# Performance work log

Measured on AMD Instinct MI355X. Metric: run time of the kernel, lower is better.

## Reference

```python
import jax, jax.numpy as jnp
import numpy as np

HIDDEN = 2048
LATENT = 512
ROPE_DIM = 64
NUM_HEADS = 16
HEAD_DIM = HIDDEN // NUM_HEADS  # 128
ROPE_THETA = 10000.0
B, S = 2, 2048


def _rope_tables(seq_len):
    # theta_i = 1 / rope_theta ** (2i / rope_dim)
    theta = 1.0 / ROPE_THETA ** (jnp.arange(0, ROPE_DIM, 2, dtype=jnp.float32) / ROPE_DIM)
    idx_theta = jnp.arange(seq_len, dtype=jnp.float32)[:, None] * theta[None, :]  # [S, rd/2]
    return jnp.cos(idx_theta), jnp.sin(idx_theta)


def _apply_rope(x, cos, sin):
    # x: [B, S, H, rd]; interleaved pairs rotated, matching the torch RoPE module.
    x2 = x.reshape(*x.shape[:-1], -1, 2)  # [B,S,H,rd/2,2]
    c = cos[None, :, None, :]
    s = sin[None, :, None, :]
    out = jnp.stack([x2[..., 0] * c - x2[..., 1] * s,
                     x2[..., 1] * c + x2[..., 0] * s], axis=-1)
    return out.reshape(x.shape)


def setup_inputs() -> dict:
    key = jax.random.key(0)
    ks = jax.random.split(key, 9)
    def lin(k, fan_in, fan_out):
        # weights stored [in, out]; y = x @ W (same math as torch Linear)
        bound = 1.0 / np.sqrt(fan_in)
        return jax.random.uniform(k, (fan_in, fan_out), jnp.float32, -bound, bound)
    return {
        "h": jax.random.normal(ks[0], (B, S, HIDDEN), jnp.float32),
        "W_DKV": lin(ks[1], HIDDEN, LATENT),
        "W_UK": lin(ks[2], LATENT, HIDDEN),
        "W_KR": lin(ks[3], HIDDEN, ROPE_DIM),
        "W_UV": lin(ks[4], LATENT, HIDDEN),
        "W_DQ": lin(ks[5], HIDDEN, LATENT),
        "W_UQ": lin(ks[6], LATENT, HIDDEN),
        "W_QR": lin(ks[7], LATENT, ROPE_DIM * NUM_HEADS),
        "W_O": lin(ks[8], HIDDEN, HIDDEN),
    }


def reference(h, W_DKV, W_UK, W_KR, W_UV, W_DQ, W_UQ, W_QR, W_O):
    b, s, _ = h.shape
    cos, sin = _rope_tables(s)

    # --- keys / values (shared latent) ---
    c_KV = h @ W_DKV                                      # [B,S,latent]
    k_C = (c_KV @ W_UK).reshape(b, s, NUM_HEADS, HEAD_DIM)
    k_R = _apply_rope((h @ W_KR)[:, :, None, :], cos, sin)  # [B,S,1,rd]
    k_R = jnp.broadcast_to(k_R, (b, s, NUM_HEADS, ROPE_DIM))
    k = jnp.concatenate([k_C, k_R], axis=-1)             # [B,S,H,hd+rd]
    v = (c_KV @ W_UV).reshape(b, s, NUM_HEADS, HEAD_DIM)

    # --- queries ---
    c_Q = h @ W_DQ                                        # [B,S,latent]
    q_C = (c_Q @ W_UQ).reshape(b, s, NUM_HEADS, HEAD_DIM)
    q_R = _apply_rope((c_Q @ W_QR).reshape(b, s, NUM_HEADS, ROPE_DIM), cos, sin)
    q = jnp.concatenate([q_C, q_R], axis=-1)             # [B,S,H,hd+rd]

    # --- attention (explicit SxS scores, causal) ---
    scale = 1.0 / np.sqrt(HEAD_DIM + ROPE_DIM)
    scores = jnp.einsum('bshd,bthd->bhst', q, k) * scale  # [B,H,S,S]
    causal = jnp.tril(jnp.ones((s, s), dtype=bool))
    scores = jnp.where(causal[None, None], scores, -jnp.inf)
    probs = jax.nn.softmax(scores, axis=-1)
    o = jnp.einsum('bhst,bthd->bshd', probs, v)           # [B,S,H,hd]

    return o.reshape(b, s, HIDDEN) @ W_O
```

## Files before the change

### kernel.cpp

```cpp
#include <hip/hip_runtime.h>
#include <hip/hip_bf16.h>
#include <type_traits>
#include <cstdint>

typedef __bf16 bf16x8 __attribute__((ext_vector_type(8)));
typedef float f32x4 __attribute__((ext_vector_type(4)));
typedef __hip_bfloat16 bf16;

static constexpr int BB = 2, SEQ = 2048, HID = 2048, LAT = 512, NHEAD = 16;
static constexpr int HD = 128, RD = 64, DQK = 192;
static constexpr int MR = BB * SEQ;
static constexpr int LDW1 = 1152;
static constexpr int LDKV = 4096;
static constexpr int LDQ3 = 3072;

__device__ __forceinline__ float bf2f(bf16 x) { return __bfloat162float(x); }
__device__ __forceinline__ bf16 f2bf(float x) { return __float2bfloat16(x); }

__device__ __forceinline__ void gload16(const void* g, void* l) {
  __builtin_amdgcn_global_load_lds(
      (__attribute__((address_space(1))) void*)(uintptr_t)g,
      (__attribute__((address_space(3))) void*)(uint32_t)(uintptr_t)l,
      16, 0, 0);
}

__global__ void k_cvt(const float* __restrict__ in, bf16* __restrict__ out, int n4) {
  int i = blockIdx.x * 256 + threadIdx.x;
  if (i >= n4) return;
  float4 v = reinterpret_cast<const float4*>(in)[i];
  bf16* o = out + (size_t)i * 4;
  o[0] = f2bf(v.x); o[1] = f2bf(v.y); o[2] = f2bf(v.z); o[3] = f2bf(v.w);
}

__global__ void k_transpose_cvt(const float* __restrict__ W, bf16* __restrict__ WT,
                                int K, int N) {
  __shared__ float t[32][33];
  int k0 = blockIdx.y * 32, n0 = blockIdx.x * 32;
  int c = threadIdx.x & 31, r0 = threadIdx.x >> 5;
#pragma unroll
  for (int i = 0; i < 32; i += 8) t[r0 + i][c] = W[(size_t)(k0 + r0 + i) * N + n0 + c];
  __syncthreads();
#pragma unroll
  for (int i = 0; i < 32; i += 8)
    WT[(size_t)(n0 + r0 + i) * K + k0 + c] = f2bf(t[c][r0 + i]);
}

__global__ void k_transpose_v(const bf16* __restrict__ kv, bf16* __restrict__ vt) {
  __shared__ bf16 t[32][34];
  int bh = blockIdx.z, b = bh >> 4, hh = bh & 15;
  int s0 = blockIdx.y * 32, d0 = blockIdx.x * 32;
  int c = threadIdx.x & 31, r0 = threadIdx.x >> 5;
#pragma unroll
  for (int i = 0; i < 32; i += 8)
    t[r0 + i][c] = kv[((size_t)b * SEQ + s0 + r0 + i) * LDKV + HID + hh * HD + d0 + c];
  __syncthreads();
#pragma unroll
  for (int i = 0; i < 32; i += 8)
    vt[((size_t)bh * HD + d0 + r0 + i) * SEQ + s0 + c] = t[c][r0 + i];
}

__global__ void k_rope_tables(float* __restrict__ cosT, float* __restrict__ sinT) {
  int idx = blockIdx.x * 256 + threadIdx.x;
  int s = idx >> 5, j = idx & 31;
  float freq = powf(10000.0f, -(float)(2 * j) / 64.0f);
  float a = (float)s * freq;
  cosT[idx] = cosf(a);
  sinT[idx] = sinf(a);
}

template <int BM, int BN, typename OutT>
__global__ __launch_bounds__((BM / 64) * (BN / 64) * 64)
void k_gemm_bt(const bf16* __restrict__ A, int lda, const bf16* __restrict__ BT,
               OutT* __restrict__ C, int ldc, int M, int N, int K) {
  constexpr int BK = 32;
  constexpr int WN = BN / 64, NW = (BM / 64) * WN;
  __shared__ alignas(16) bf16 As[BM * BK];
  __shared__ alignas(16) bf16 Bs[BN * BK];
  const int tid = threadIdx.x, wave = tid >> 6, lane = tid & 63;
  const int lr = lane & 15, lk = lane >> 4;
  const int wm = (wave / WN) * 64, wn = (wave % WN) * 64;
  const int m0 = blockIdx.y * BM, n0 = blockIdx.x * BN;
  const int srow = lane >> 2;
  const int scol = (lane & 3) * 8;
  f32x4 acc[4][4] = {};
  for (int kt = 0; kt < K; kt += BK) {
    for (int c = wave; c < BM / 16; c += NW)
      gload16(A + (size_t)(m0 + c * 16 + srow) * lda + kt + scol, (char*)As + c * 1024);
    for (int c = wave; c < BN / 16; c += NW)
      gload16(BT + (size_t)(n0 + c * 16 + srow) * K + kt + scol, (char*)Bs + c * 1024);
    __syncthreads();
    bf16x8 af[4], bfr[4];
#pragma unroll
    for (int i = 0; i < 4; i++)
      af[i] = *reinterpret_cast<const bf16x8*>(As + (wm + i * 16 + lr) * BK + lk * 8);
#pragma unroll
    for (int j = 0; j < 4; j++)
      bfr[j] = *reinterpret_cast<const bf16x8*>(Bs + (wn + j * 16 + lr) * BK + lk * 8);
    __builtin_amdgcn_s_setprio(1);
#pragma unroll
    for (int i = 0; i < 4; i++)
#pragma unroll
      for (int j = 0; j < 4; j++)
        acc[i][j] = __builtin_amdgcn_mfma_f32_16x16x32_bf16(af[i], bfr[j], acc[i][j], 0, 0, 0);
    __builtin_amdgcn_s_setprio(0);
    __syncthreads();
  }
#pragma unroll
  for (int i = 0; i < 4; i++)
#pragma unroll
    for (int j = 0; j < 4; j++) {
      int row = m0 + wm + i * 16 + lk * 4, col = n0 + wn + j * 16 + lr;
#pragma unroll
      for (int r = 0; r < 4; r++) {
        float v = acc[i][j][r];
        if constexpr (std::is_same<OutT, float>::value)
          C[(size_t)(row + r) * ldc + col] = v;
        else
          C[(size_t)(row + r) * ldc + col] = f2bf(v);
      }
    }
}

__global__ void k_assemble_q(const bf16* __restrict__ q3,
                             const float* __restrict__ cosT, const float* __restrict__ sinT,
                             bf16* __restrict__ qbuf) {
  size_t idx = (size_t)blockIdx.x * 256 + threadIdx.x;
  int d = (int)(idx % DQK);
  size_t t = idx / DQK;
  int s = (int)(t % SEQ); t /= SEQ;
  int hh = (int)(t % NHEAD);
  int b = (int)(t / NHEAD);
  size_t row = (size_t)b * SEQ + s;
  bf16 v;
  if (d < HD) {
    v = q3[row * LDQ3 + hh * HD + d];
  } else {
    int dd = d - HD, j = dd >> 1;
    float cs = cosT[s * 32 + j], sn = sinT[s * 32 + j];
    float x0 = bf2f(q3[row * LDQ3 + HID + hh * RD + 2 * j]);
    float x1 = bf2f(q3[row * LDQ3 + HID + hh * RD + 2 * j + 1]);
    v = f2bf((dd & 1) ? (x1 * cs + x0 * sn) : (x0 * cs - x1 * sn));
  }
  qbuf[idx] = v;
}

__global__ void k_assemble_k(const bf16* __restrict__ kv, const bf16* __restrict__ out1,
                             const float* __restrict__ cosT, const float* __restrict__ sinT,
                             bf16* __restrict__ kbuf) {
  size_t idx = (size_t)blockIdx.x * 256 + threadIdx.x;
  int d = (int)(idx % DQK);
  size_t t = idx / DQK;
  int s = (int)(t % SEQ); t /= SEQ;
  int hh = (int)(t % NHEAD);
  int b = (int)(t / NHEAD);
  size_t row = (size_t)b * SEQ + s;
  bf16 v;
  if (d < HD) {
    v = kv[row * LDKV + hh * HD + d];
  } else {
    int dd = d - HD, j = dd >> 1;
    float cs = cosT[s * 32 + j], sn = sinT[s * 32 + j];
    float x0 = bf2f(out1[row * LDW1 + 1024 + 2 * j]);
    float x1 = bf2f(out1[row * LDW1 + 1024 + 2 * j + 1]);
    v = f2bf((dd & 1) ? (x1 * cs + x0 * sn) : (x0 * cs - x1 * sn));
  }
  kbuf[idx] = v;
}

__global__ __launch_bounds__(256)
void k_attn(const bf16* __restrict__ Q, const bf16* __restrict__ Kb,
            const bf16* __restrict__ VT, bf16* __restrict__ Of) {
  constexpr int QB = 64, KBL = 64;
  __shared__ alignas(16) bf16 Ks[KBL * DQK];
  __shared__ alignas(16) bf16 Vs[HD * KBL];
  __shared__ alignas(16) bf16 Ps[4 * 16 * KBL];
  const int qt = (SEQ / QB - 1) - (blockIdx.x >> 5);
  const int bh = blockIdx.x & 31;
  const int b = bh >> 4, hh = bh & 15;
  const int tid = threadIdx.x, wave = tid >> 6, lane = tid & 63;
  const int lr = lane & 15, lk = lane >> 4;
  const int q0 = qt * QB;
  const float scale = 0.07216878364870323f;

  const bf16* Qp = Q + ((size_t)bh * SEQ + q0 + wave * 16 + lr) * DQK;
  bf16x8 qf[6];
#pragma unroll
  for (int c = 0; c < 6; c++)
    qf[c] = *reinterpret_cast<const bf16x8*>(Qp + c * 32 + lk * 8);

  bf16* PsW = Ps + wave * (16 * KBL);

  f32x4 oacc[8] = {};
  float mrow[4], lrow[4];
#pragma unroll
  for (int r = 0; r < 4; r++) { mrow[r] = -INFINITY; lrow[r] = 0.f; }

  for (int kt = 0; kt <= qt; kt++) {
    const int k0 = kt * KBL;
    const bf16* Kbase = Kb + ((size_t)bh * SEQ + k0) * DQK;
    const bf16* Vbase = VT + (size_t)bh * HD * SEQ + k0;
    for (int c = wave; c < 24; c += 4) {
      int S = c * 64 + lane;
      int row = S / 24;
      int scl = (S - row * 24) ^ (row & 7);
      gload16(Kbase + row * DQK + scl * 8, (char*)Ks + c * 1024);
    }
    for (int c = wave; c < 16; c += 4) {
      int S = c * 64 + lane;
      int row = S >> 3;
      int scl = (S & 7) ^ (row & 7);
      gload16(Vbase + (size_t)row * SEQ + scl * 8, (char*)Vs + c * 1024);
    }
    __syncthreads();

    f32x4 sc[4] = {};
    __builtin_amdgcn_s_setprio(1);
#pragma unroll
    for (int cb = 0; cb < 4; cb++) {
      const int krow = cb * 16 + lr;
#pragma unroll
      for (int c = 0; c < 6; c++) {
        int phys = (c * 4 + lk) ^ (krow & 7);
        bf16x8 kf = *reinterpret_cast<const bf16x8*>(Ks + krow * DQK + phys * 8);
        sc[cb] = __builtin_amdgcn_mfma_f32_16x16x32_bf16(qf[c], kf, sc[cb], 0, 0, 0);
      }
    }
    __builtin_amdgcn_s_setprio(0);

    const bool maskit = (kt == qt);
    float p[4][4], tm[4];
#pragma unroll
    for (int r = 0; r < 4; r++) tm[r] = -INFINITY;
#pragma unroll
    for (int cb = 0; cb < 4; cb++) {
      const int kcg = k0 + cb * 16 + lr;
#pragma unroll
      for (int r = 0; r < 4; r++) {
        float v = sc[cb][r] * scale;
        if (maskit && kcg > q0 + wave * 16 + lk * 4 + r) v = -INFINITY;
        p[cb][r] = v;
        tm[r] = fmaxf(tm[r], v);
      }
    }
#pragma unroll
    for (int m = 1; m < 16; m <<= 1)
#pragma unroll
      for (int r = 0; r < 4; r++) tm[r] = fmaxf(tm[r], __shfl_xor(tm[r], m, 16));

    float rs[4];
#pragma unroll
    for (int r = 0; r < 4; r++) {
      float mn = fmaxf(mrow[r], tm[r]);
      float al = __expf(mrow[r] - mn);
      mrow[r] = mn;
      lrow[r] *= al;
#pragma unroll
      for (int ocb = 0; ocb < 8; ocb++) oacc[ocb][r] *= al;
      float ssum = 0.f;
#pragma unroll
      for (int cb = 0; cb < 4; cb++) {
        float e = __expf(p[cb][r] - mn);
        p[cb][r] = e;
        ssum += e;
      }
      rs[r] = ssum;
    }
#pragma unroll
    for (int m = 1; m < 16; m <<= 1)
#pragma unroll
      for (int r = 0; r < 4; r++) rs[r] += __shfl_xor(rs[r], m, 16);
#pragma unroll
    for (int r = 0; r < 4; r++) lrow[r] += rs[r];

#pragma unroll
    for (int cb = 0; cb < 4; cb++)
#pragma unroll
      for (int r = 0; r < 4; r++) {
        int prow = lk * 4 + r;
        int pslot = (cb * 2 + (lr >> 3)) ^ (prow & 7);
        PsW[prow * KBL + pslot * 8 + (lr & 7)] = f2bf(p[cb][r]);
      }

    __builtin_amdgcn_s_setprio(1);
#pragma unroll
    for (int kk = 0; kk < 2; kk++) {
      int pphys = (kk * 4 + lk) ^ (lr & 7);
      bf16x8 pa = *reinterpret_cast<const bf16x8*>(PsW + lr * KBL + pphys * 8);
#pragma unroll
      for (int ocb = 0; ocb < 8; ocb++) {
        int vrow = ocb * 16 + lr;
        int vphys = (kk * 4 + lk) ^ (vrow & 7);
        bf16x8 vb = *reinterpret_cast<const bf16x8*>(Vs + vrow * KBL + vphys * 8);
        oacc[ocb] = __builtin_amdgcn_mfma_f32_16x16x32_bf16(pa, vb, oacc[ocb], 0, 0, 0);
      }
    }
    __builtin_amdgcn_s_setprio(0);
    __syncthreads();
  }

#pragma unroll
  for (int ocb = 0; ocb < 8; ocb++)
#pragma unroll
    for (int r = 0; r < 4; r++) {
      int qr = q0 + wave * 16 + lk * 4 + r;
      float v = oacc[ocb][r] / lrow[r];
      Of[((size_t)b * SEQ + qr) * HID + hh * HD + ocb * 16 + lr] = f2bf(v);
    }
}

extern "C" void kernel_launch(void* const* d_in, const int* in_sizes, int n_in,
                              void* d_out, int out_size, void* d_ws, size_t ws_size,
                              hipStream_t stream) {
  const float* h    = (const float*)d_in[0];
  const float* Wdkv = (const float*)d_in[1];
  const float* Wuk  = (const float*)d_in[2];
  const float* Wkr  = (const float*)d_in[3];
  const float* Wuv  = (const float*)d_in[4];
  const float* Wdq  = (const float*)d_in[5];
  const float* Wuq  = (const float*)d_in[6];
  const float* Wqr  = (const float*)d_in[7];
  const float* Wo   = (const float*)d_in[8];
  float* out = (float*)d_out;

  char* w = (char*)d_ws;
  auto alloc = [&](size_t elems) {
    bf16* p = (bf16*)w;
    w += (elems * sizeof(bf16) + 255) & ~(size_t)255;
    return p;
  };
  bf16* hb   = alloc((size_t)MR * HID);
  bf16* wt1  = alloc((size_t)LDW1 * HID);
  bf16* wt2  = alloc((size_t)LDKV * LAT);
  bf16* wt3  = alloc((size_t)LDQ3 * LAT);
  bf16* woT  = alloc((size_t)HID * HID);
  bf16* out1 = alloc((size_t)MR * LDW1);
  bf16* kv   = alloc((size_t)MR * LDKV);
  bf16* q3   = alloc((size_t)MR * LDQ3);
  bf16* qbuf = alloc((size_t)BB * NHEAD * SEQ * DQK);
  bf16* kbuf = alloc((size_t)BB * NHEAD * SEQ * DQK);
  bf16* vt   = alloc((size_t)BB * NHEAD * HD * SEQ);
  bf16* oflat= alloc((size_t)MR * HID);
  float* cosT = (float*)alloc((size_t)SEQ * 32 * 2);
  float* sinT = (float*)alloc((size_t)SEQ * 32 * 2);

  k_cvt<<<MR * HID / 4 / 256, 256, 0, stream>>>(h, hb, MR * HID / 4);
  k_transpose_cvt<<<dim3(512 / 32, HID / 32), 256, 0, stream>>>(Wdkv, wt1, HID, 512);
  k_transpose_cvt<<<dim3(512 / 32, HID / 32), 256, 0, stream>>>(Wdq, wt1 + (size_t)512 * HID, HID, 512);
  k_transpose_cvt<<<dim3(RD / 32, HID / 32), 256, 0, stream>>>(Wkr, wt1 + (size_t)1024 * HID, HID, RD);
  k_transpose_cvt<<<dim3(HID / 32, LAT / 32), 256, 0, stream>>>(Wuk, wt2, LAT, HID);
  k_transpose_cvt<<<dim3(HID / 32, LAT / 32), 256, 0, stream>>>(Wuv, wt2 + (size_t)HID * LAT, LAT, HID);
  k_transpose_cvt<<<dim3(HID / 32, LAT / 32), 256, 0, stream>>>(Wuq, wt3, LAT, HID);
  k_transpose_cvt<<<dim3(RD * NHEAD / 32, LAT / 32), 256, 0, stream>>>(Wqr, wt3 + (size_t)HID * LAT, LAT, RD * NHEAD);
  k_transpose_cvt<<<dim3(HID / 32, HID / 32), 256, 0, stream>>>(Wo, woT, HID, HID);
  k_rope_tables<<<SEQ * 32 / 256, 256, 0, stream>>>(cosT, sinT);

  k_gemm_bt<128, 128, bf16><<<dim3(LDW1 / 128, MR / 128), 256, 0, stream>>>(hb, HID, wt1, out1, LDW1, MR, LDW1, HID);
  k_gemm_bt<128, 128, bf16><<<dim3(LDKV / 128, MR / 128), 256, 0, stream>>>(out1, LDW1, wt2, kv, LDKV, MR, LDKV, LAT);
  k_gemm_bt<128, 128, bf16><<<dim3(LDQ3 / 128, MR / 128), 256, 0, stream>>>(out1 + 512, LDW1, wt3, q3, LDQ3, MR, LDQ3, LAT);

  unsigned qblocks = (unsigned)((size_t)BB * NHEAD * SEQ * DQK / 256);
  k_assemble_q<<<qblocks, 256, 0, stream>>>(q3, cosT, sinT, qbuf);
  k_assemble_k<<<qblocks, 256, 0, stream>>>(kv, out1, cosT, sinT, kbuf);
  k_transpose_v<<<dim3(HD / 32, SEQ / 32, BB * NHEAD), 256, 0, stream>>>(kv, vt);

  k_attn<<<(SEQ / 64) * 32, 256, 0, stream>>>(qbuf, kbuf, vt, oflat);

  k_gemm_bt<128, 128, float><<<dim3(HID / 128, MR / 128), 256, 0, stream>>>(oflat, HID, woT, out, HID, MR, HID, HID);
}
```

Baseline: 470.0 us.

## Merge prep/assemble launches, fuse kv/q GEMMs, pair causal q-tiles in attention

Folds the weight transposes, h conversion and rope table build into one prep kernel, and merges the two latent-up GEMMs into one launch. Q/K assembly plus the V transpose become a single kernel with 8-wide vector loads and stores. The attention kernel now gives each block two query tiles, one early and one late, so causal work is balanced across blocks and each loaded K/V tile is used twice. It also skips the softmax rescale when the running max does not change. This cuts launch count and load imbalance at the cost of more registers in attention (two sets of accumulators) and fewer attention blocks.

```diff
diff --git a/kernel.cpp b/kernel.cpp
--- a/kernel.cpp
+++ b/kernel.cpp
@@ -24,54 +24,58 @@
       16, 0, 0);
 }
 
-__global__ void k_cvt(const float* __restrict__ in, bf16* __restrict__ out, int n4) {
-  int i = blockIdx.x * 256 + threadIdx.x;
-  if (i >= n4) return;
-  float4 v = reinterpret_cast<const float4*>(in)[i];
-  bf16* o = out + (size_t)i * 4;
-  o[0] = f2bf(v.x); o[1] = f2bf(v.y); o[2] = f2bf(v.z); o[3] = f2bf(v.w);
-}
-
-__global__ void k_transpose_cvt(const float* __restrict__ W, bf16* __restrict__ WT,
-                                int K, int N) {
-  __shared__ float t[32][33];
-  int k0 = blockIdx.y * 32, n0 = blockIdx.x * 32;
+__global__ void k_prep(const float* __restrict__ h,
+                       const float* __restrict__ Wdkv, const float* __restrict__ Wdq,
+                       const float* __restrict__ Wkr, const float* __restrict__ Wuk,
+                       const float* __restrict__ Wuv, const float* __restrict__ Wuq,
+                       const float* __restrict__ Wqr, const float* __restrict__ Wo,
+                       bf16* __restrict__ hb, bf16* __restrict__ wt1, bf16* __restrict__ wt2,
+                       bf16* __restrict__ wt3, bf16* __restrict__ woT,
+                       float* __restrict__ cosT, float* __restrict__ sinT) {
+  __shared__ float tbuf[32][33];
+  int blk = blockIdx.x;
+  if (blk >= 10112) {
+    int i = (blk - 10112) * 256 + threadIdx.x;
+    float4 v = reinterpret_cast<const float4*>(h)[i];
+    bf16* o = hb + (size_t)i * 4;
+    o[0] = f2bf(v.x); o[1] = f2bf(v.y); o[2] = f2bf(v.z); o[3] = f2bf(v.w);
+    return;
+  }
+  if (blk >= 9856) {
+    int idx = (blk - 9856) * 256 + threadIdx.x;
+    int s = idx >> 5, j = idx & 31;
+    float freq = powf(10000.0f, -(float)(2 * j) / 64.0f);
+    float a = (float)s * freq;
+    cosT[idx] = cosf(a);
+    sinT[idx] = sinf(a);
+    return;
+  }
+  const float* src; bf16* dst; int K, N, local;
+  if (blk < 1024)      { src = Wdkv; dst = wt1;                      K = 2048; N = 512;  local = blk; }
+  else if (blk < 2048) { src = Wdq;  dst = wt1 + (size_t)512 * 2048; K = 2048; N = 512;  local = blk - 1024; }
+  else if (blk < 2176) { src = Wkr;  dst = wt1 + (size_t)1024 * 2048;K = 2048; N = 64;   local = blk - 2048; }
+  else if (blk < 3200) { src = Wuk;  dst = wt2;                      K = 512;  N = 2048; local = blk - 2176; }
+  else if (blk < 4224) { src = Wuv;  dst = wt2 + (size_t)2048 * 512; K = 512;  N = 2048; local = blk - 3200; }
+  else if (blk < 5248) { src = Wuq;  dst = wt3;                      K = 512;  N = 2048; local = blk - 4224; }
+  else if (blk < 5760) { src = Wqr;  dst = wt3 + (size_t)2048 * 512; K = 512;  N = 1024; local = blk - 5248; }
+  else                 { src = Wo;   dst = woT;                      K = 2048; N = 2048; local = blk - 5760; }
+  int tilesX = N >> 5;
+  int tx = local % tilesX, ty = local / tilesX;
+  int k0 = ty * 32, n0 = tx * 32;
   int c = threadIdx.x & 31, r0 = threadIdx.x >> 5;
 #pragma unroll
-  for (int i = 0; i < 32; i += 8) t[r0 + i][c] = W[(size_t)(k0 + r0 + i) * N + n0 + c];
+  for (int i = 0; i < 32; i += 8) tbuf[r0 + i][c] = src[(size_t)(k0 + r0 + i) * N + n0 + c];
   __syncthreads();
 #pragma unroll
   for (int i = 0; i < 32; i += 8)
-    WT[(size_t)(n0 + r0 + i) * K + k0 + c] = f2bf(t[c][r0 + i]);
-}
-
-__global__ void k_transpose_v(const bf16* __restrict__ kv, bf16* __restrict__ vt) {
-  __shared__ bf16 t[32][34];
-  int bh = blockIdx.z, b = bh >> 4, hh = bh & 15;
-  int s0 = blockIdx.y * 32, d0 = blockIdx.x * 32;
-  int c = threadIdx.x & 31, r0 = threadIdx.x >> 5;
-#pragma unroll
-  for (int i = 0; i < 32; i += 8)
-    t[r0 + i][c] = kv[((size_t)b * SEQ + s0 + r0 + i) * LDKV + HID + hh * HD + d0 + c];
-  __syncthreads();
-#pragma unroll
-  for (int i = 0; i < 32; i += 8)
-    vt[((size_t)bh * HD + d0 + r0 + i) * SEQ + s0 + c] = t[c][r0 + i];
-}
-
-__global__ void k_rope_tables(float* __restrict__ cosT, float* __restrict__ sinT) {
-  int idx = blockIdx.x * 256 + threadIdx.x;
-  int s = idx >> 5, j = idx & 31;
-  float freq = powf(10000.0f, -(float)(2 * j) / 64.0f);
-  float a = (float)s * freq;
-  cosT[idx] = cosf(a);
-  sinT[idx] = sinf(a);
+    dst[(size_t)(n0 + r0 + i) * K + k0 + c] = f2bf(tbuf[c][r0 + i]);
 }
 
 template <int BM, int BN, typename OutT>
-__global__ __launch_bounds__((BM / 64) * (BN / 64) * 64)
-void k_gemm_bt(const bf16* __restrict__ A, int lda, const bf16* __restrict__ BT,
-               OutT* __restrict__ C, int ldc, int M, int N, int K) {
+__device__ __forceinline__ void gemm_body(const bf16* __restrict__ A, int lda,
+                                          const bf16* __restrict__ BT,
+                                          OutT* __restrict__ C, int ldc, int K,
+                                          int m0, int n0) {
   constexpr int BK = 32;
   constexpr int WN = BN / 64, NW = (BM / 64) * WN;
   __shared__ alignas(16) bf16 As[BM * BK];
@@ -79,7 +83,6 @@
   const int tid = threadIdx.x, wave = tid >> 6, lane = tid & 63;
   const int lr = lane & 15, lk = lane >> 4;
   const int wm = (wave / WN) * 64, wn = (wave % WN) * 64;
-  const int m0 = blockIdx.y * BM, n0 = blockIdx.x * BN;
   const int srow = lane >> 2;
   const int scol = (lane & 3) * 8;
   f32x4 acc[4][4] = {};
@@ -121,81 +124,211 @@
     }
 }
 
-__global__ void k_assemble_q(const bf16* __restrict__ q3,
-                             const float* __restrict__ cosT, const float* __restrict__ sinT,
-                             bf16* __restrict__ qbuf) {
-  size_t idx = (size_t)blockIdx.x * 256 + threadIdx.x;
-  int d = (int)(idx % DQK);
-  size_t t = idx / DQK;
-  int s = (int)(t % SEQ); t /= SEQ;
-  int hh = (int)(t % NHEAD);
-  int b = (int)(t / NHEAD);
-  size_t row = (size_t)b * SEQ + s;
-  bf16 v;
-  if (d < HD) {
-    v = q3[row * LDQ3 + hh * HD + d];
-  } else {
-    int dd = d - HD, j = dd >> 1;
-    float cs = cosT[s * 32 + j], sn = sinT[s * 32 + j];
-    float x0 = bf2f(q3[row * LDQ3 + HID + hh * RD + 2 * j]);
-    float x1 = bf2f(q3[row * LDQ3 + HID + hh * RD + 2 * j + 1]);
-    v = f2bf((dd & 1) ? (x1 * cs + x0 * sn) : (x0 * cs - x1 * sn));
-  }
-  qbuf[idx] = v;
-}
-
-__global__ void k_assemble_k(const bf16* __restrict__ kv, const bf16* __restrict__ out1,
-                             const float* __restrict__ cosT, const float* __restrict__ sinT,
-                             bf16* __restrict__ kbuf) {
-  size_t idx = (size_t)blockIdx.x * 256 + threadIdx.x;
-  int d = (int)(idx % DQK);
-  size_t t = idx / DQK;
-  int s = (int)(t % SEQ); t /= SEQ;
-  int hh = (int)(t % NHEAD);
-  int b = (int)(t / NHEAD);
-  size_t row = (size_t)b * SEQ + s;
-  bf16 v;
-  if (d < HD) {
-    v = kv[row * LDKV + hh * HD + d];
-  } else {
-    int dd = d - HD, j = dd >> 1;
-    float cs = cosT[s * 32 + j], sn = sinT[s * 32 + j];
-    float x0 = bf2f(out1[row * LDW1 + 1024 + 2 * j]);
-    float x1 = bf2f(out1[row * LDW1 + 1024 + 2 * j + 1]);
-    v = f2bf((dd & 1) ? (x1 * cs + x0 * sn) : (x0 * cs - x1 * sn));
-  }
-  kbuf[idx] = v;
+template <int BM, int BN, typename OutT>
+__global__ __launch_bounds__(256)
+void k_gemm_bt(const bf16* __restrict__ A, int lda, const bf16* __restrict__ BT,
+               OutT* __restrict__ C, int ldc, int K) {
+  gemm_body<BM, BN, OutT>(A, lda, BT, C, ldc, K, blockIdx.y * BM, blockIdx.x * BN);
+}
+
+__global__ __launch_bounds__(256)
+void k_gemm23(const bf16* __restrict__ out1, const bf16* __restrict__ wt2,
+              const bf16* __restrict__ wt3, bf16* __restrict__ kv, bf16* __restrict__ q3) {
+  int n0g = blockIdx.x * 128, m0 = blockIdx.y * 128;
+  const bf16* A; const bf16* BT; bf16* C; int ldc, n0;
+  if (n0g < LDKV) { A = out1;       BT = wt2; C = kv; ldc = LDKV; n0 = n0g; }
+  else            { A = out1 + 512; BT = wt3; C = q3; ldc = LDQ3; n0 = n0g - LDKV; }
+  gemm_body<128, 128, bf16>(A, LDW1, BT, C, ldc, LAT, m0, n0);
+}
+
+__device__ __forceinline__ bf16x8 rope8(bf16x8 x, float4 c4, float4 s4) {
+  bf16x8 o;
+  float cp[4] = {c4.x, c4.y, c4.z, c4.w};
+  float sp[4] = {s4.x, s4.y, s4.z, s4.w};
+#pragma unroll
+  for (int pe = 0; pe < 4; pe++) {
+    float x0 = (float)x[2 * pe], x1 = (float)x[2 * pe + 1];
+    o[2 * pe]     = (__bf16)(x0 * cp[pe] - x1 * sp[pe]);
+    o[2 * pe + 1] = (__bf16)(x1 * cp[pe] + x0 * sp[pe]);
+  }
+  return o;
+}
+
+__global__ void k_assemble(const bf16* __restrict__ q3, const bf16* __restrict__ kv,
+                           const bf16* __restrict__ out1,
+                           const float* __restrict__ cosT, const float* __restrict__ sinT,
+                           bf16* __restrict__ qbuf, bf16* __restrict__ kbuf,
+                           bf16* __restrict__ vt) {
+  __shared__ bf16 tv[32][34];
+  int blk = blockIdx.x;
+  if (blk < 12288) {
+    bool isQ = blk < 6144;
+    int gid = (isQ ? blk : blk - 6144) * 256 + threadIdx.x;
+    int rowIdx = gid / 24, pos = gid - rowIdx * 24;
+    int d8 = pos * 8;
+    int s = rowIdx & (SEQ - 1);
+    int bhh = rowIdx >> 11;
+    int hh = bhh & 15, b = bhh >> 4;
+    size_t row = (size_t)b * SEQ + s;
+    bf16x8 o;
+    if (isQ) {
+      if (d8 < HD) {
+        o = *reinterpret_cast<const bf16x8*>(&q3[row * LDQ3 + hh * HD + d8]);
+      } else {
+        int dd8 = d8 - HD;
+        bf16x8 x = *reinterpret_cast<const bf16x8*>(&q3[row * LDQ3 + HID + hh * RD + dd8]);
+        float4 c4 = *reinterpret_cast<const float4*>(&cosT[s * 32 + (dd8 >> 1)]);
+        float4 s4 = *reinterpret_cast<const float4*>(&sinT[s * 32 + (dd8 >> 1)]);
+        o = rope8(x, c4, s4);
+      }
+      *reinterpret_cast<bf16x8*>(&qbuf[(size_t)gid * 8]) = o;
+    } else {
+      if (d8 < HD) {
+        o = *reinterpret_cast<const bf16x8*>(&kv[row * LDKV + hh * HD + d8]);
+      } else {
+        int dd8 = d8 - HD;
+        bf16x8 x = *reinterpret_cast<const bf16x8*>(&out1[row * LDW1 + 1024 + dd8]);
+        float4 c4 = *reinterpret_cast<const float4*>(&cosT[s * 32 + (dd8 >> 1)]);
+        float4 s4 = *reinterpret_cast<const float4*>(&sinT[s * 32 + (dd8 >> 1)]);
+        o = rope8(x, c4, s4);
+      }
+      *reinterpret_cast<bf16x8*>(&kbuf[(size_t)gid * 8]) = o;
+    }
+    return;
+  }
+  int local = blk - 12288;
+  int dx = local & 3, sy = (local >> 2) & 63, bh = local >> 8;
+  int b = bh >> 4, hh = bh & 15;
+  int s0 = sy * 32, d0 = dx * 32;
+  int c = threadIdx.x & 31, r0 = threadIdx.x >> 5;
+#pragma unroll
+  for (int i = 0; i < 32; i += 8)
+    tv[r0 + i][c] = kv[((size_t)b * SEQ + s0 + r0 + i) * LDKV + HID + hh * HD + d0 + c];
+  __syncthreads();
+#pragma unroll
+  for (int i = 0; i < 32; i += 8)
+    vt[((size_t)bh * HD + d0 + r0 + i) * SEQ + s0 + c] = tv[c][r0 + i];
 }
 
 __global__ __launch_bounds__(256)
 void k_attn(const bf16* __restrict__ Q, const bf16* __restrict__ Kb,
             const bf16* __restrict__ VT, bf16* __restrict__ Of) {
-  constexpr int QB = 64, KBL = 64;
+  constexpr int KBL = 64, NT = SEQ / 64;
   __shared__ alignas(16) bf16 Ks[KBL * DQK];
   __shared__ alignas(16) bf16 Vs[HD * KBL];
   __shared__ alignas(16) bf16 Ps[4 * 16 * KBL];
-  const int qt = (SEQ / QB - 1) - (blockIdx.x >> 5);
-  const int bh = blockIdx.x & 31;
+  const int nid = (blockIdx.x & 7) * 64 + (blockIdx.x >> 3);
+  const int bh = nid >> 4, pid = nid & 15;
+  const int qtA = pid, qtB = NT - 1 - pid;
   const int b = bh >> 4, hh = bh & 15;
   const int tid = threadIdx.x, wave = tid >> 6, lane = tid & 63;
   const int lr = lane & 15, lk = lane >> 4;
-  const int q0 = qt * QB;
+  const int rb = wave * 16 + lk * 4;
   const float scale = 0.07216878364870323f;
 
-  const bf16* Qp = Q + ((size_t)bh * SEQ + q0 + wave * 16 + lr) * DQK;
-  bf16x8 qf[6];
-#pragma unroll
-  for (int c = 0; c < 6; c++)
-    qf[c] = *reinterpret_cast<const bf16x8*>(Qp + c * 32 + lk * 8);
+  bf16x8 qf[2][6];
+#pragma unroll
+  for (int t = 0; t < 2; t++) {
+    int q0 = (t ? qtB : qtA) * 64;
+    const bf16* Qp = Q + ((size_t)bh * SEQ + q0 + wave * 16 + lr) * DQK;
+#pragma unroll
+    for (int c = 0; c < 6; c++)
+      qf[t][c] = *reinterpret_cast<const bf16x8*>(Qp + c * 32 + lk * 8);
+  }
 
   bf16* PsW = Ps + wave * (16 * KBL);
-
-  f32x4 oacc[8] = {};
-  float mrow[4], lrow[4];
-#pragma unroll
-  for (int r = 0; r < 4; r++) { mrow[r] = -INFINITY; lrow[r] = 0.f; }
-
-  for (int kt = 0; kt <= qt; kt++) {
+  f32x4 oacc[2][8] = {};
+  float mrow[2][4], lrow[2][4];
+#pragma unroll
+  for (int t = 0; t < 2; t++)
+#pragma unroll
+    for (int r = 0; r < 4; r++) { mrow[t][r] = -INFINITY; lrow[t][r] = 0.f; }
+
+  auto proc = [&](auto tc, bool maskit, int k0, int q0) {
+    constexpr int t = decltype(tc)::value;
+    f32x4 sc[4] = {};
+    __builtin_amdgcn_s_setprio(1);
+#pragma unroll
+    for (int cb = 0; cb < 4; cb++) {
+      const int krow = cb * 16 + lr;
+#pragma unroll
+      for (int c = 0; c < 6; c++) {
+        int phys = (c * 4 + lk) ^ (krow & 7);
+        bf16x8 kf = *reinterpret_cast<const bf16x8*>(Ks + krow * DQK + phys * 8);
+        sc[cb] = __builtin_amdgcn_mfma_f32_16x16x32_bf16(qf[t][c], kf, sc[cb], 0, 0, 0);
+      }
+    }
+    __builtin_amdgcn_s_setprio(0);
+    float p[4][4], tm[4];
+#pragma unroll
+    for (int r = 0; r < 4; r++) tm[r] = -INFINITY;
+#pragma unroll
+    for (int cb = 0; cb < 4; cb++) {
+      const int kcg = k0 + cb * 16 + lr;
+#pragma unroll
+      for (int r = 0; r < 4; r++) {
+        float v = sc[cb][r] * scale;
+        if (maskit && kcg > q0 + rb + r) v = -INFINITY;
+        p[cb][r] = v;
+        tm[r] = fmaxf(tm[r], v);
+      }
+    }
+#pragma unroll
+    for (int m = 1; m < 16; m <<= 1)
+#pragma unroll
+      for (int r = 0; r < 4; r++) tm[r] = fmaxf(tm[r], __shfl_xor(tm[r], m, 16));
+    float rs[4];
+#pragma unroll
+    for (int r = 0; r < 4; r++) {
+      float mo = mrow[t][r];
+      float mn = fmaxf(mo, tm[r]);
+      if (tm[r] > mo) {
+        float al = __expf(mo - mn);
+        mrow[t][r] = mn;
+        lrow[t][r] *= al;
+#pragma unroll
+        for (int ocb = 0; ocb < 8; ocb++) oacc[t][ocb][r] *= al;
+      }
+      float ssum = 0.f;
+#pragma unroll
+      for (int cb = 0; cb < 4; cb++) {
+        float e = __expf(p[cb][r] - mn);
+        p[cb][r] = e;
+        ssum += e;
+      }
+      rs[r] = ssum;
+    }
+#pragma unroll
+    for (int m = 1; m < 16; m <<= 1)
+#pragma unroll
+      for (int r = 0; r < 4; r++) rs[r] += __shfl_xor(rs[r], m, 16);
+#pragma unroll
+    for (int r = 0; r < 4; r++) lrow[t][r] += rs[r];
+#pragma unroll
+    for (int cb = 0; cb < 4; cb++)
+#pragma unroll
+      for (int r = 0; r < 4; r++) {
+        int prow = lk * 4 + r;
+        int pslot = (cb * 2 + (lr >> 3)) ^ (prow & 7);
+        PsW[prow * KBL + pslot * 8 + (lr & 7)] = f2bf(p[cb][r]);
+      }
+    __builtin_amdgcn_s_setprio(1);
+#pragma unroll
+    for (int kk = 0; kk < 2; kk++) {
+      int pphys = (kk * 4 + lk) ^ (lr & 7);
+      bf16x8 pa = *reinterpret_cast<const bf16x8*>(PsW + lr * KBL + pphys * 8);
+#pragma unroll
+      for (int ocb = 0; ocb < 8; ocb++) {
+        int vrow = ocb * 16 + lr;
+        int vphys = (kk * 4 + lk) ^ (vrow & 7);
+        bf16x8 vb = *reinterpret_cast<const bf16x8*>(Vs + vrow * KBL + vphys * 8);
+        oacc[t][ocb] = __builtin_amdgcn_mfma_f32_16x16x32_bf16(pa, vb, oacc[t][ocb], 0, 0, 0);
+      }
+    }
+    __builtin_amdgcn_s_setprio(0);
+  };
+
+  for (int kt = 0; kt <= qtB; kt++) {
     const int k0 = kt * KBL;
     const bf16* Kbase = Kb + ((size_t)bh * SEQ + k0) * DQK;
     const bf16* Vbase = VT + (size_t)bh * HD * SEQ + k0;
@@ -212,100 +345,23 @@
       gload16(Vbase + (size_t)row * SEQ + scl * 8, (char*)Vs + c * 1024);
     }
     __syncthreads();
-
-    f32x4 sc[4] = {};
-    __builtin_amdgcn_s_setprio(1);
-#pragma unroll
-    for (int cb = 0; cb < 4; cb++) {
-      const int krow = cb * 16 + lr;
-#pragma unroll
-      for (int c = 0; c < 6; c++) {
-        int phys = (c * 4 + lk) ^ (krow & 7);
-        bf16x8 kf = *reinterpret_cast<const bf16x8*>(Ks + krow * DQK + phys * 8);
-        sc[cb] = __builtin_amdgcn_mfma_f32_16x16x32_bf16(qf[c], kf, sc[cb], 0, 0, 0);
-      }
-    }
-    __builtin_amdgcn_s_setprio(0);
-
-    const bool maskit = (kt == qt);
-    float p[4][4], tm[4];
-#pragma unroll
-    for (int r = 0; r < 4; r++) tm[r] = -INFINITY;
-#pragma unroll
-    for (int cb = 0; cb < 4; cb++) {
-      const int kcg = k0 + cb * 16 + lr;
+    proc(std::integral_constant<int, 1>{}, kt == qtB, k0, qtB * 64);
+    if (kt <= qtA) proc(std::integral_constant<int, 0>{}, kt == qtA, k0, qtA * 64);
+    __syncthreads();
+  }
+
+#pragma unroll
+  for (int t = 0; t < 2; t++) {
+    int q0 = (t ? qtB : qtA) * 64;
+#pragma unroll
+    for (int ocb = 0; ocb < 8; ocb++)
 #pragma unroll
       for (int r = 0; r < 4; r++) {
-        float v = sc[cb][r] * scale;
-        if (maskit && kcg > q0 + wave * 16 + lk * 4 + r) v = -INFINITY;
-        p[cb][r] = v;
-        tm[r] = fmaxf(tm[r], v);
-      }
-    }
-#pragma unroll
-    for (int m = 1; m < 16; m <<= 1)
-#pragma unroll
-      for (int r = 0; r < 4; r++) tm[r] = fmaxf(tm[r], __shfl_xor(tm[r], m, 16));
-
-    float rs[4];
-#pragma unroll
-    for (int r = 0; r < 4; r++) {
-      float mn = fmaxf(mrow[r], tm[r]);
-      float al = __expf(mrow[r] - mn);
-      mrow[r] = mn;
-      lrow[r] *= al;
-#pragma unroll
-      for (int ocb = 0; ocb < 8; ocb++) oacc[ocb][r] *= al;
-      float ssum = 0.f;
-#pragma unroll
-      for (int cb = 0; cb < 4; cb++) {
-        float e = __expf(p[cb][r] - mn);
-        p[cb][r] = e;
-        ssum += e;
-      }
-      rs[r] = ssum;
-    }
-#pragma unroll
-    for (int m = 1; m < 16; m <<= 1)
-#pragma unroll
-      for (int r = 0; r < 4; r++) rs[r] += __shfl_xor(rs[r], m, 16);
-#pragma unroll
-    for (int r = 0; r < 4; r++) lrow[r] += rs[r];
-
-#pragma unroll
-    for (int cb = 0; cb < 4; cb++)
-#pragma unroll
-      for (int r = 0; r < 4; r++) {
-        int prow = lk * 4 + r;
-        int pslot = (cb * 2 + (lr >> 3)) ^ (prow & 7);
-        PsW[prow * KBL + pslot * 8 + (lr & 7)] = f2bf(p[cb][r]);
-      }
-
-    __builtin_amdgcn_s_setprio(1);
-#pragma unroll
-    for (int kk = 0; kk < 2; kk++) {
-      int pphys = (kk * 4 + lk) ^ (lr & 7);
-      bf16x8 pa = *reinterpret_cast<const bf16x8*>(PsW + lr * KBL + pphys * 8);
-#pragma unroll
-      for (int ocb = 0; ocb < 8; ocb++) {
-        int vrow = ocb * 16 + lr;
-        int vphys = (kk * 4 + lk) ^ (vrow & 7);
-        bf16x8 vb = *reinterpret_cast<const bf16x8*>(Vs + vrow * KBL + vphys * 8);
-        oacc[ocb] = __builtin_amdgcn_mfma_f32_16x16x32_bf16(pa, vb, oacc[ocb], 0, 0, 0);
-      }
-    }
-    __builtin_amdgcn_s_setprio(0);
-    __syncthreads();
-  }
-
-#pragma unroll
-  for (int ocb = 0; ocb < 8; ocb++)
-#pragma unroll
-    for (int r = 0; r < 4; r++) {
-      int qr = q0 + wave * 16 + lk * 4 + r;
-      float v = oacc[ocb][r] / lrow[r];
-      Of[((size_t)b * SEQ + qr) * HID + hh * HD + ocb * 16 + lr] = f2bf(v);
-    }
+        int qr = q0 + rb + r;
+        float v = oacc[t][ocb][r] / lrow[t][r];
+        Of[((size_t)b * SEQ + qr) * HID + hh * HD + ocb * 16 + lr] = f2bf(v);
+      }
+  }
 }
 
 extern "C" void kernel_launch(void* const* d_in, const int* in_sizes, int n_in,
@@ -343,27 +399,11 @@
   float* cosT = (float*)alloc((size_t)SEQ * 32 * 2);
   float* sinT = (float*)alloc((size_t)SEQ * 32 * 2);
 
-  k_cvt<<<MR * HID / 4 / 256, 256, 0, stream>>>(h, hb, MR * HID / 4);
-  k_transpose_cvt<<<dim3(512 / 32, HID / 32), 256, 0, stream>>>(Wdkv, wt1, HID, 512);
-  k_transpose_cvt<<<dim3(512 / 32, HID / 32), 256, 0, stream>>>(Wdq, wt1 + (size_t)512 * HID, HID, 512);
-  k_transpose_cvt<<<dim3(RD / 32, HID / 32), 256, 0, stream>>>(Wkr, wt1 + (size_t)1024 * HID, HID, RD);
-  k_transpose_cvt<<<dim3(HID / 32, LAT / 32), 256, 0, stream>>>(Wuk, wt2, LAT, HID);
-  k_transpose_cvt<<<dim3(HID / 32, LAT / 32), 256, 0, stream>>>(Wuv, wt2 + (size_t)HID * LAT, LAT, HID);
-  k_transpose_cvt<<<dim3(HID / 32, LAT / 32), 256, 0, stream>>>(Wuq, wt3, LAT, HID);
-  k_transpose_cvt<<<dim3(RD * NHEAD / 32, LAT / 32), 256, 0, stream>>>(Wqr, wt3 + (size_t)HID * LAT, LAT, RD * NHEAD);
-  k_transpose_cvt<<<dim3(HID / 32, HID / 32), 256, 0, stream>>>(Wo, woT, HID, HID);
-  k_rope_tables<<<SEQ * 32 / 256, 256, 0, stream>>>(cosT, sinT);
-
-  k_gemm_bt<128, 128, bf16><<<dim3(LDW1 / 128, MR / 128), 256, 0, stream>>>(hb, HID, wt1, out1, LDW1, MR, LDW1, HID);
-  k_gemm_bt<128, 128, bf16><<<dim3(LDKV / 128, MR / 128), 256, 0, stream>>>(out1, LDW1, wt2, kv, LDKV, MR, LDKV, LAT);
-  k_gemm_bt<128, 128, bf16><<<dim3(LDQ3 / 128, MR / 128), 256, 0, stream>>>(out1 + 512, LDW1, wt3, q3, LDQ3, MR, LDQ3, LAT);
-
-  unsigned qblocks = (unsigned)((size_t)BB * NHEAD * SEQ * DQK / 256);
-  k_assemble_q<<<qblocks, 256, 0, stream>>>(q3, cosT, sinT, qbuf);
-  k_assemble_k<<<qblocks, 256, 0, stream>>>(kv, out1, cosT, sinT, kbuf);
-  k_transpose_v<<<dim3(HD / 32, SEQ / 32, BB * NHEAD), 256, 0, stream>>>(kv, vt);
-
-  k_attn<<<(SEQ / 64) * 32, 256, 0, stream>>>(qbuf, kbuf, vt, oflat);
-
-  k_gemm_bt<128, 128, float><<<dim3(HID / 128, MR / 128), 256, 0, stream>>>(oflat, HID, woT, out, HID, MR, HID, HID);
-}
+  k_prep<<<18304, 256, 0, stream>>>(h, Wdkv, Wdq, Wkr, Wuk, Wuv, Wuq, Wqr, Wo,
+                                    hb, wt1, wt2, wt3, woT, cosT, sinT);
+  k_gemm_bt<128, 128, bf16><<<dim3(LDW1 / 128, MR / 128), 256, 0, stream>>>(hb, HID, wt1, out1, LDW1, HID);
+  k_gemm23<<<dim3((LDKV + LDQ3) / 128, MR / 128), 256, 0, stream>>>(out1, wt2, wt3, kv, q3);
+  k_assemble<<<20480, 256, 0, stream>>>(q3, kv, out1, cosT, sinT, qbuf, kbuf, vt);
+  k_attn<<<512, 256, 0, stream>>>(qbuf, kbuf, vt, oflat);
+  k_gemm_bt<128, 128, float><<<dim3(HID / 128, MR / 128), 256, 0, stream>>>(oflat, HID, woT, out, HID, HID);
+}
```

New measurement: 501.3 us. 1.07x slower.
